# Kernel optimization log

Hardware: AMD Instinct MI355X
Metric: run time of the kernel (lower is better)

## Reference

```python
import jax, jax.numpy as jnp
import numpy as np

B, C, H, W = 512, 1, 128, 128
RS, WS = 12, 12
L, HID, T = 128, 512, 16


def setup_inputs() -> dict:
    key = jax.random.key(0)
    ks = jax.random.split(key, 24)

    def u(k, shape, fan):
        return jax.random.uniform(k, shape, jnp.float32, -1.0, 1.0) / np.sqrt(fan)

    enc_in = 2 * RS * RS + HID  # 800
    inp = {
        "x": jax.random.uniform(ks[0], (B, C, H, W), jnp.float32),
        "eps": jax.random.normal(ks[1], (T, B, L), jnp.float32),
        "glimpses": T,
        "canvas_init": jnp.zeros((C, H, W), jnp.float32),
        "h_dec_init": jnp.zeros((HID,), jnp.float32),
        "h_enc_init": jnp.zeros((HID,), jnp.float32),
        "W_ih_enc": u(ks[2], (4 * HID, enc_in), enc_in),
        "b_ih_enc": u(ks[3], (4 * HID,), enc_in),
        "W_hh_enc": u(ks[4], (4 * HID, HID), HID),
        "b_hh_enc": u(ks[5], (4 * HID,), HID),
        "W_ih_dec": u(ks[6], (4 * HID, L), L),
        "b_ih_dec": u(ks[7], (4 * HID,), L),
        "W_hh_dec": u(ks[8], (4 * HID, HID), HID),
        "b_hh_dec": u(ks[9], (4 * HID,), HID),
        "W_samp": u(ks[10], (2 * L, HID), HID),
        "b_samp": u(ks[11], (2 * L,), HID),
        "W_rattn": u(ks[12], (5, HID), HID),
        "b_rattn": u(ks[13], (5,), HID),
        "W_wattn": u(ks[14], (5, HID), HID),
        "b_wattn": u(ks[15], (5,), HID),
        "W_writer": u(ks[16], (WS * WS, HID), HID),
        "b_writer": u(ks[17], (WS * WS,), HID),
    }
    return inp


def _lstm_cell(x, h, c, Wih, bih, Whh, bhh):
    gates = x @ Wih.T + bih + h @ Whh.T + bhh
    i, f, g, o = jnp.split(gates, 4, axis=-1)
    c_new = jax.nn.sigmoid(f) * c + jax.nn.sigmoid(i) * jnp.tanh(g)
    h_new = jax.nn.sigmoid(o) * jnp.tanh(c_new)
    return h_new, c_new


def _filter_bank(gx, gy, variance, stride, size):
    # gx, gy, variance, stride: [B,1]
    offsets = (jnp.arange(size, dtype=jnp.float32) + 0.5 - size / 2) * stride  # [B,size]
    mu_x = (gx + offsets)[..., None]  # [B,size,1]
    mu_y = (gy + offsets)[..., None]
    var = variance[:, :, None]  # [B,1,1]
    a = jnp.arange(W, dtype=jnp.float32)
    b = jnp.arange(H, dtype=jnp.float32)
    Fx = jnp.exp(-((a - mu_x) ** 2) / (2 * var))  # [B,size,W]
    Fy = jnp.exp(-((b - mu_y) ** 2) / (2 * var))  # [B,size,H]
    Fx = Fx / jnp.maximum(Fx.sum(axis=2, keepdims=True), 1e-8)
    Fy = Fy / jnp.maximum(Fy.sum(axis=2, keepdims=True), 1e-8)
    return Fx, Fy


def _attn_window(h_state, Wattn, battn, size):
    res = h_state @ Wattn.T + battn  # [B,5]
    gx_, gy_, log_var, log_delta, log_inten = [res[:, i:i + 1] for i in range(5)]
    gx = (W + 1) * (gx_ + 1) / 2
    gy = (H + 1) * (gy_ + 1) / 2
    stride = (max(H, W) - 1) * jnp.exp(log_delta) / (size - 1)
    Fx, Fy = _filter_bank(gx, gy, jnp.exp(log_var), stride, size)
    return Fx, Fy, jnp.exp(log_inten)


def _read(x, x_error, h_dec, W_rattn, b_rattn):
    Fx, Fy, inten = _attn_window(h_dec, W_rattn, b_rattn, RS)
    FxT = jnp.swapaxes(Fx, -1, -2)[:, None]  # [B,1,W,RS]
    Fy = Fy[:, None]  # [B,1,RS,H]
    glimpse = jnp.concatenate((Fy @ x @ FxT, Fy @ x_error @ FxT), axis=1)  # [B,2C,RS,RS]
    return inten[:, :, None, None] * glimpse


def _write(h_dec, W_writer, b_writer, W_wattn, b_wattn):
    w = (h_dec @ W_writer.T + b_writer).reshape(-1, C, WS, WS)
    Fx, Fy, inten = _attn_window(h_dec, W_wattn, b_wattn, WS)
    FyT = jnp.swapaxes(Fy, -1, -2)[:, None]  # [B,1,H,WS]
    Fx = Fx[:, None]  # [B,1,WS,W]
    return (FyT @ w @ Fx) / inten[:, :, None, None]  # [B,C,H,W]


def reference(x, eps, glimpses, canvas_init, h_dec_init, h_enc_init,
              W_ih_enc, b_ih_enc, W_hh_enc, b_hh_enc,
              W_ih_dec, b_ih_dec, W_hh_dec, b_hh_dec,
              W_samp, b_samp, W_rattn, b_rattn, W_wattn, b_wattn,
              W_writer, b_writer):
    batch = x.shape[0]
    canvas0 = jnp.broadcast_to(canvas_init, (batch, C, H, W))
    h_dec0 = jnp.broadcast_to(h_dec_init, (batch, HID))
    h_enc0 = jnp.broadcast_to(h_enc_init, (batch, HID))
    c0 = jnp.zeros((batch, HID), x.dtype)

    def step(carry, eps_t):
        canvas, h_enc, c_enc, h_dec, c_dec = carry
        x_error = x - jax.nn.sigmoid(canvas)
        r = _read(x, x_error, h_dec, W_rattn, b_rattn).reshape(batch, -1)
        enc_in = jnp.concatenate((r, h_dec), axis=1)
        h_enc, c_enc = _lstm_cell(enc_in, h_enc, c_enc, W_ih_enc, b_ih_enc, W_hh_enc, b_hh_enc)
        s = h_enc @ W_samp.T + b_samp
        mu, log_var = s[:, :L], s[:, L:]
        z = mu + jnp.exp(log_var * 0.5) * eps_t
        h_dec, c_dec = _lstm_cell(z, h_dec, c_dec, W_ih_dec, b_ih_dec, W_hh_dec, b_hh_dec)
        canvas = canvas + _write(h_dec, W_writer, b_writer, W_wattn, b_wattn)
        return (canvas, h_enc, c_enc, h_dec, c_dec), (mu, log_var)

    (canvas, _, _, _, _), (mus, log_vars) = jax.lax.scan(
        step, (canvas0, h_enc0, c0, h_dec0, c0), eps[:glimpses])
    # mus/log_vars: [T,B,L] -> [B,T,L] to match torch.stack(mu, dim=1)
    return jax.nn.sigmoid(canvas), jnp.swapaxes(mus, 0, 1), jnp.swapaxes(log_vars, 0, 1)
```

## Files before the change

kernel.cpp:

```cpp
#include <hip/hip_runtime.h>
#include <hip/hip_bf16.h>
#include <math.h>

#define BATCH 512
#define HID 512
#define LAT 128
#define TSTEPS 16
#define IMG 16384
#define ENC_IN 800
#define GATES 2048

#define SEC_E 1344
#define SEC_D 640

typedef __attribute__((ext_vector_type(8))) short short8;
typedef __attribute__((ext_vector_type(4))) float f32x4;

__device__ __forceinline__ void gload16(const void* g, void* l) {
    __builtin_amdgcn_global_load_lds((const __attribute__((address_space(1))) unsigned int*)g,
                                     (__attribute__((address_space(3))) unsigned int*)l, 16, 0, 0);
}

__device__ __forceinline__ void bsplit(float v, unsigned short& hi, unsigned short& lo) {
    unsigned u = __float_as_uint(v);
    unsigned uh = (u + (0x7FFFu + ((u >> 16) & 1u))) & 0xFFFF0000u;
    hi = (unsigned short)(uh >> 16);
    float r = v - __uint_as_float(uh);
    unsigned ur = __float_as_uint(r);
    unsigned ul = (ur + (0x7FFFu + ((ur >> 16) & 1u))) & 0xFFFF0000u;
    lo = (unsigned short)(ul >> 16);
}

__global__ __launch_bounds__(256) void init_canvas(float* __restrict__ canvas,
                                                   const float* __restrict__ ci) {
    int idx = blockIdx.x * 256 + threadIdx.x;
    canvas[idx] = ci[idx & (IMG - 1)];
}

__global__ __launch_bounds__(256) void init_state(float* __restrict__ he, float* __restrict__ ce,
                                                  float* __restrict__ hd, float* __restrict__ cd,
                                                  const float* __restrict__ hei,
                                                  const float* __restrict__ hdi,
                                                  unsigned short* __restrict__ A_enc,
                                                  unsigned short* __restrict__ A_dec) {
    int idx = blockIdx.x * 256 + threadIdx.x;
    int b = idx >> 9, u = idx & 511;
    float ve = hei[u], vd = hdi[u];
    he[idx] = ve;
    hd[idx] = vd;
    ce[idx] = 0.f;
    cd[idx] = 0.f;
    unsigned short hi, lo;
    bsplit(ve, hi, lo);
    size_t be = (size_t)b * 2 * SEC_E;
    A_enc[be + 800 + u] = hi;
    A_enc[be + SEC_E + 800 + u] = lo;
    bsplit(vd, hi, lo);
    size_t bd = (size_t)b * 2 * SEC_D;
    A_dec[bd + 128 + u] = hi;
    A_dec[bd + SEC_D + 128 + u] = lo;
}

__global__ __launch_bounds__(256) void sigmoid_final(float* __restrict__ c) {
    int idx = blockIdx.x * 256 + threadIdx.x;
    c[idx] = 1.f / (1.f + expf(-c[idx]));
}

__global__ __launch_bounds__(256) void prep_wsplit(const float* __restrict__ W1, int K1,
                                                   const float* __restrict__ W2, int K2,
                                                   unsigned short* __restrict__ out, int SEC) {
    int kk = blockIdx.x * 256 + threadIdx.x;
    int n = blockIdx.y;
    if (kk >= SEC) return;
    float v = 0.f;
    if (kk < K1) v = W1[(size_t)n * K1 + kk];
    else if (kk < K1 + K2) v = W2[(size_t)n * K2 + (kk - K1)];
    unsigned short hi, lo;
    bsplit(v, hi, lo);
    size_t base = (size_t)n * 2 * SEC;
    out[base + kk] = hi;
    out[base + SEC + kk] = lo;
}

__global__ __launch_bounds__(256) void gemm_bf16x3(const unsigned short* __restrict__ Au,
                                                   const unsigned short* __restrict__ Wu,
                                                   float* __restrict__ C, int SEC,
                                                   int ktb0, int kte0, int ktb1, int kte1) {
    __shared__ __align__(16) char lds[2][16384];
    const __bf16* A = (const __bf16*)Au;
    const __bf16* Wt = (const __bf16*)Wu;
    const int ld = 2 * SEC;
    const int tid = threadIdx.x;
    const int z = blockIdx.z;
    const int bm = blockIdx.x * 64;
    const int bn = blockIdx.y * 64;
    const int ktb = z ? ktb1 : ktb0;
    const int kte = z ? kte1 : kte0;

    const int row0 = tid >> 3, c0 = tid & 7;
    const size_t ga0 = (size_t)(bm + row0) * ld + (size_t)((c0 ^ (row0 & 7)) * 8);
    const size_t ga1 = ga0 + (size_t)32 * ld;
    const size_t gb0 = (size_t)(bn + row0) * ld + (size_t)((c0 ^ (row0 & 7)) * 8);
    const size_t gb1 = gb0 + (size_t)32 * ld;
    const int lA0 = tid * 16, lA1 = (tid + 256) * 16;
    const int lB0 = 8192 + tid * 16, lB1 = 8192 + (tid + 256) * 16;

    const int lane = tid & 63, wv = tid >> 6;
    const int rA = wv * 16 + (lane & 15);
    const int chnk = (lane >> 4) ^ (lane & 7);
    const int byteA = rA * 128 + chnk * 16;
    const int byteB = 8192 + (lane & 15) * 128 + chnk * 16;

    f32x4 acc[4];
#pragma unroll
    for (int j = 0; j < 4; ++j) acc[j] = (f32x4){0.f, 0.f, 0.f, 0.f};

    auto STAGE = [&](int buf, int kt) {
        const int kw = kt * 64;
        const int ka = (kw >= SEC) ? (kw - SEC) : kw;
        const int kb = (kw >= 2 * SEC) ? (kw - 2 * SEC) : kw;
        const __bf16* a = A + ka;
        const __bf16* w = Wt + kb;
        char* l = &lds[buf][0];
        gload16(a + ga0, l + lA0);
        gload16(a + ga1, l + lA1);
        gload16(w + gb0, l + lB0);
        gload16(w + gb1, l + lB1);
    };

    STAGE(0, ktb);
    asm volatile("s_waitcnt vmcnt(0)" ::: "memory");
    __syncthreads();
    int buf = 0;
    for (int kt = ktb; kt < kte; ++kt) {
        if (kt + 1 < kte) STAGE(buf ^ 1, kt + 1);
        const char* base = &lds[buf][0];
        short8 a0 = *(const short8*)(base + byteA);
        short8 a1 = *(const short8*)(base + (byteA ^ 64));
#pragma unroll
        for (int j = 0; j < 4; ++j) {
            short8 b0 = *(const short8*)(base + (byteB + j * 2048));
            short8 b1 = *(const short8*)(base + ((byteB + j * 2048) ^ 64));
            acc[j] = __builtin_amdgcn_mfma_f32_16x16x32_bf16(a0, b0, acc[j], 0, 0, 0);
            acc[j] = __builtin_amdgcn_mfma_f32_16x16x32_bf16(a1, b1, acc[j], 0, 0, 0);
        }
        asm volatile("s_waitcnt vmcnt(0)" ::: "memory");
        __syncthreads();
        buf ^= 1;
    }
    float* Cz = C + (size_t)z * BATCH * GATES;
    const int crow = bm + wv * 16 + (lane >> 4) * 4;
    const int ccol = bn + (lane & 15);
#pragma unroll
    for (int j = 0; j < 4; ++j)
#pragma unroll
        for (int r = 0; r < 4; ++r)
            Cz[(size_t)(crow + r) * GATES + ccol + j * 16] = acc[j][r];
}

__global__ __launch_bounds__(512, 4) void read_glimpse_fused(const float* __restrict__ x,
                                                             const float* __restrict__ canvas,
                                                             const float* __restrict__ h_dec,
                                                             const float* __restrict__ Wa,
                                                             const float* __restrict__ ba,
                                                             unsigned short* __restrict__ A_enc) {
    const int b = blockIdx.x, t = threadIdx.x;
    __shared__ float par[5];
    __shared__ float fx[12][132], fy[12][132];
    __shared__ float dn[24];
    __shared__ float tm[12][132], te[12][132];
    __shared__ __align__(16) float pbuf[8][12][128];
    float* red = &pbuf[0][0][0];
    const float* hb = h_dec + (size_t)b * HID;
#pragma unroll
    for (int j = 0; j < 5; ++j) red[j * 512 + t] = hb[t] * Wa[j * HID + t];
    __syncthreads();
    for (int o = 256; o > 0; o >>= 1) {
        if (t < o) {
#pragma unroll
            for (int j = 0; j < 5; ++j) red[j * 512 + t] += red[j * 512 + t + o];
        }
        __syncthreads();
    }
    if (t < 5) par[t] = red[t * 512] + ba[t];
    __syncthreads();
    const float gx = 129.f * (par[0] + 1.f) * 0.5f;
    const float gy = 129.f * (par[1] + 1.f) * 0.5f;
    const float var = expf(par[2]);
    const float strd = 127.f * expf(par[3]) / 11.f;
    const float iv = expf(par[4]);
#pragma unroll
    for (int rep = 0; rep < 6; ++rep) {
        int e = t + rep * 512;
        int mat = e / 1536;
        int rr = (e - mat * 1536) >> 7;
        int cc = e & 127;
        float ctr = (mat ? gy : gx) + ((float)rr + 0.5f - 6.f) * strd;
        float d = (float)cc - ctr;
        float v = expf(-(d * d) / (2.f * var));
        float (*dst)[132] = mat ? fy : fx;
        dst[rr][cc] = v;
    }
    __syncthreads();
    if (t < 24) {
        const float (*src)[132] = (t < 12) ? fx : fy;
        int rr = (t < 12) ? t : t - 12;
        float s = 0.f;
        for (int k = 0; k < 128; ++k) s += src[rr][k];
        dn[t] = fmaxf(s, 1e-8f);
    }
    __syncthreads();
#pragma unroll
    for (int rep = 0; rep < 6; ++rep) {
        int e = t + rep * 512;
        int mat = e / 1536;
        int rr = (e - mat * 1536) >> 7;
        int cc = e & 127;
        float (*dst)[132] = mat ? fy : fx;
        dst[rr][cc] /= dn[mat * 12 + rr];
    }
    __syncthreads();
    const int g = t >> 6, l = t & 63, c2 = l * 2;
    float2 am[12] = {}, ae[12] = {};
    const float* xb = x + (size_t)b * IMG;
    const float* cb = canvas + (size_t)b * IMG;
    for (int hh = g * 16; hh < g * 16 + 16; ++hh) {
        float2 xv = *(const float2*)(xb + hh * 128 + c2);
        float2 cv = *(const float2*)(cb + hh * 128 + c2);
        float2 xe;
        xe.x = xv.x - 1.f / (1.f + expf(-cv.x));
        xe.y = xv.y - 1.f / (1.f + expf(-cv.y));
#pragma unroll
        for (int i = 0; i < 12; ++i) {
            float f = fy[i][hh];
            am[i].x += f * xv.x;
            am[i].y += f * xv.y;
            ae[i].x += f * xe.x;
            ae[i].y += f * xe.y;
        }
    }
#pragma unroll
    for (int i = 0; i < 12; ++i) *(float2*)(&pbuf[g][i][c2]) = am[i];
    __syncthreads();
    for (int it = t; it < 1536; it += 512) {
        int ii = it >> 7, cc = it & 127;
        float s = 0.f;
#pragma unroll
        for (int k = 0; k < 8; ++k) s += pbuf[k][ii][cc];
        tm[ii][cc] = s;
    }
    __syncthreads();
#pragma unroll
    for (int i = 0; i < 12; ++i) *(float2*)(&pbuf[g][i][c2]) = ae[i];
    __syncthreads();
    for (int it = t; it < 1536; it += 512) {
        int ii = it >> 7, cc = it & 127;
        float s = 0.f;
#pragma unroll
        for (int k = 0; k < 8; ++k) s += pbuf[k][ii][cc];
        te[ii][cc] = s;
    }
    __syncthreads();
    unsigned short hi, lo;
    unsigned short* rb = A_enc + (size_t)b * 2 * SEC_E;
    if (t < 288) {
        int ch = (t >= 144) ? 1 : 0;
        int rem = t - ch * 144;
        int ii = rem / 12, jj = rem - ii * 12;
        const float* src = ch ? te[ii] : tm[ii];
        float s = 0.f;
        for (int w2 = 0; w2 < 128; ++w2) s += src[w2] * fx[jj][w2];
        bsplit(iv * s, hi, lo);
        rb[t] = hi;
        rb[SEC_E + t] = lo;
    }
    bsplit(hb[t], hi, lo);
    rb[288 + t] = hi;
    rb[SEC_E + 288 + t] = lo;
    if (t < 32) {
        rb[1312 + t] = 0;
        rb[SEC_E + 1312 + t] = 0;
    }
}

template <int TM, int TN>
__global__ __launch_bounds__(256) void gemm_slab(const float* __restrict__ A0,
                                                 const float* __restrict__ W0,
                                                 const float* __restrict__ bias0, int ld0, int K0,
                                                 const float* __restrict__ A1,
                                                 const float* __restrict__ W1,
                                                 const float* __restrict__ bias1, int ld1, int K1,
                                                 float* __restrict__ C, int M, int N) {
    constexpr int BM = 16 * TM, BN = 16 * TN, BK = 16;
    __shared__ float As[BK][BM + 4];
    __shared__ float Ws[BK][BN + 4];
    const int z = blockIdx.z;
    const float* A = z ? A1 : A0;
    const float* Wm = z ? W1 : W0;
    const float* bs = z ? bias1 : bias0;
    const int ld = z ? ld1 : ld0;
    const int K = z ? K1 : K0;
    const int tid = threadIdx.x;
    const int tx = tid & 15, ty = tid >> 4;
    const int bm = blockIdx.x * BM, bn = blockIdx.y * BN;
    float acc[TM][TN] = {};
    for (int k0 = 0; k0 < K; k0 += BK) {
        __syncthreads();
        for (int i = tid; i < BM * 4; i += 256) {
            int row = i >> 2, c4 = i & 3;
            const float4 v = *(const float4*)(A + (size_t)(bm + row) * ld + k0 + c4 * 4);
            As[c4 * 4 + 0][row] = v.x;
            As[c4 * 4 + 1][row] = v.y;
            As[c4 * 4 + 2][row] = v.z;
            As[c4 * 4 + 3][row] = v.w;
        }
        for (int i = tid; i < BN * 4; i += 256) {
            int row = i >> 2, c4 = i & 3;
            int wr = bn + row;
            float4 v = make_float4(0.f, 0.f, 0.f, 0.f);
            if (wr < N) v = *(const float4*)(Wm + (size_t)wr * ld + k0 + c4 * 4);
            Ws[c4 * 4 + 0][row] = v.x;
            Ws[c4 * 4 + 1][row] = v.y;
            Ws[c4 * 4 + 2][row] = v.z;
            Ws[c4 * 4 + 3][row] = v.w;
        }
        __syncthreads();
#pragma unroll
        for (int c = 0; c < BK; ++c) {
            float a[TM], w[TN];
#pragma unroll
            for (int i = 0; i < TM; ++i) a[i] = As[c][ty * TM + i];
#pragma unroll
            for (int j = 0; j < TN; ++j) w[j] = Ws[c][tx * TN + j];
#pragma unroll
            for (int i = 0; i < TM; ++i)
#pragma unroll
                for (int j = 0; j < TN; ++j) acc[i][j] += a[i] * w[j];
        }
    }
    float* Cz = C + (size_t)z * M * N;
#pragma unroll
    for (int i = 0; i < TM; ++i) {
        const int rr = bm + ty * TM + i;
#pragma unroll
        for (int j = 0; j < TN; ++j) {
            const int cc = bn + tx * TN + j;
            if (cc < N) Cz[(size_t)rr * N + cc] = acc[i][j] + (bs ? bs[cc] : 0.f);
        }
    }
}

__global__ __launch_bounds__(256) void lstm_pw(const float* __restrict__ g0,
                                               const float* __restrict__ g1,
                                               const float* __restrict__ bih,
                                               const float* __restrict__ bhh,
                                               float* __restrict__ h, float* __restrict__ c,
                                               unsigned short* __restrict__ split_out,
                                               int soff, int SEC2) {
    int idx = blockIdx.x * 256 + threadIdx.x;
    int b = idx >> 9, u = idx & 511;
    size_t base = (size_t)b * GATES;
    float gi = g0[base + u] + g1[base + u] + bih[u] + bhh[u];
    float gf = g0[base + 512 + u] + g1[base + 512 + u] + bih[512 + u] + bhh[512 + u];
    float gg = g0[base + 1024 + u] + g1[base + 1024 + u] + bih[1024 + u] + bhh[1024 + u];
    float go = g0[base + 1536 + u] + g1[base + 1536 + u] + bih[1536 + u] + bhh[1536 + u];
    float si = 1.f / (1.f + expf(-gi));
    float sf = 1.f / (1.f + expf(-gf));
    float so = 1.f / (1.f + expf(-go));
    float cn = sf * c[idx] + si * tanhf(gg);
    c[idx] = cn;
    float hn = so * tanhf(cn);
    h[idx] = hn;
    unsigned short hi, lo;
    bsplit(hn, hi, lo);
    size_t sb = (size_t)b * 2 * SEC2;
    split_out[sb + soff + u] = hi;
    split_out[sb + SEC2 + soff + u] = lo;
}

__global__ __launch_bounds__(256) void z_kernel(const float* __restrict__ s,
                                                const float* __restrict__ eps_t,
                                                unsigned short* __restrict__ A_dec,
                                                float* __restrict__ mu_out,
                                                float* __restrict__ lv_out, int t) {
    int idx = blockIdx.x * 256 + threadIdx.x;
    int b = idx >> 7, l = idx & 127;
    int i0 = b * 256 + l;
    float mu = s[i0] + s[131072 + i0];
    float lv = s[i0 + 128] + s[131072 + i0 + 128];
    float zv = mu + expf(0.5f * lv) * eps_t[idx];
    unsigned short hi, lo;
    bsplit(zv, hi, lo);
    size_t bd = (size_t)b * 2 * SEC_D;
    A_dec[bd + l] = hi;
    A_dec[bd + SEC_D + l] = lo;
    size_t o = (size_t)b * (TSTEPS * LAT) + t * LAT + l;
    mu_out[o] = mu;
    lv_out[o] = lv;
}

__global__ __launch_bounds__(512, 4) void write_canvas_fused(float* __restrict__ canvas,
                                                             const float* __restrict__ h_dec,
                                                             const float* __restrict__ Wr,
                                                             const float* __restrict__ bwr,
                                                             const float* __restrict__ Wa,
                                                             const float* __restrict__ ba) {
    const int b = blockIdx.x, t = threadIdx.x;
    __shared__ float par[5];
    __shared__ float hl[512];
    __shared__ float red[5][512];
    __shared__ float fx[12][132], fyl[12][132];
    __shared__ float dn[24];
    __shared__ float wl[144];
    __shared__ float tl[128][13];
    const float* hb = h_dec + (size_t)b * HID;
    hl[t] = hb[t];
    __syncthreads();
#pragma unroll
    for (int j = 0; j < 5; ++j) red[j][t] = hl[t] * Wa[j * HID + t];
    __syncthreads();
    for (int o = 256; o > 0; o >>= 1) {
        if (t < o) {
#pragma unroll
            for (int j = 0; j < 5; ++j) red[j][t] += red[j][t + o];
        }
        __syncthreads();
    }
    if (t < 5) par[t] = red[t][0] + ba[t];
    __syncthreads();
    const float gx = 129.f * (par[0] + 1.f) * 0.5f;
    const float gy = 129.f * (par[1] + 1.f) * 0.5f;
    const float var = expf(par[2]);
    const float strd = 127.f * expf(par[3]) / 11.f;
    const float riv = 1.f / expf(par[4]);
#pragma unroll
    for (int rep = 0; rep < 6; ++rep) {
        int e = t + rep * 512;
        int mat = e / 1536;
        int rr = (e - mat * 1536) >> 7;
        int cc = e & 127;
        float ctr = (mat ? gy : gx) + ((float)rr + 0.5f - 6.f) * strd;
        float d = (float)cc - ctr;
        float v = expf(-(d * d) / (2.f * var));
        float (*dst)[132] = mat ? fyl : fx;
        dst[rr][cc] = v;
    }
    {
        const int wv = t >> 6, l = t & 63;
#pragma unroll
        for (int oi = 0; oi < 18; ++oi) {
            int o = wv * 18 + oi;
            float p = 0.f;
#pragma unroll
            for (int j = 0; j < 8; ++j) p += hl[l + 64 * j] * Wr[(size_t)o * 512 + l + 64 * j];
#pragma unroll
            for (int m = 32; m; m >>= 1) p += __shfl_xor(p, m, 64);
            if (l == 0) wl[o] = p + bwr[o];
        }
    }
    __syncthreads();
    if (t < 24) {
        const float (*src)[132] = (t < 12) ? fx : fyl;
        int rr = (t < 12) ? t : t - 12;
        float s = 0.f;
        for (int k = 0; k < 128; ++k) s += src[rr][k];
        dn[t] = fmaxf(s, 1e-8f);
    }
    __syncthreads();
#pragma unroll
    for (int rep = 0; rep < 6; ++rep) {
        int e = t + rep * 512;
        int mat = e / 1536;
        int rr = (e - mat * 1536) >> 7;
        int cc = e & 127;
        float (*dst)[132] = mat ? fyl : fx;
        dst[rr][cc] /= dn[mat * 12 + rr];
    }
    __syncthreads();
    if (t < 128) {
        float tj[12] = {};
#pragma unroll
        for (int i = 0; i < 12; ++i) {
            float f = fyl[i][t];
#pragma unroll
            for (int j = 0; j < 12; ++j) tj[j] += f * wl[i * 12 + j];
        }
#pragma unroll
        for (int j = 0; j < 12; ++j) tl[t][j] = tj[j];
    }
    __syncthreads();
    const int g = t >> 6, l = t & 63, c2 = l * 2;
    float* cb = canvas + (size_t)b * IMG;
    for (int hh = g * 16; hh < g * 16 + 16; ++hh) {
        float sx = 0.f, sy = 0.f;
#pragma unroll
        for (int j = 0; j < 12; ++j) {
            float tv = tl[hh][j];
            sx += tv * fx[j][c2];
            sy += tv * fx[j][c2 + 1];
        }
        float2 cv = *(float2*)(cb + hh * 128 + c2);
        cv.x += sx * riv;
        cv.y += sy * riv;
        *(float2*)(cb + hh * 128 + c2) = cv;
    }
}

extern "C" void kernel_launch(void* const* d_in, const int* in_sizes, int n_in,
                              void* d_out, int out_size, void* d_ws, size_t ws_size,
                              hipStream_t stream) {
    const float* x = (const float*)d_in[0];
    const float* eps = (const float*)d_in[1];
    const float* canvas_init = (const float*)d_in[3];
    const float* h_dec_init = (const float*)d_in[4];
    const float* h_enc_init = (const float*)d_in[5];
    const float* W_ih_enc = (const float*)d_in[6];
    const float* b_ih_enc = (const float*)d_in[7];
    const float* W_hh_enc = (const float*)d_in[8];
    const float* b_hh_enc = (const float*)d_in[9];
    const float* W_ih_dec = (const float*)d_in[10];
    const float* b_ih_dec = (const float*)d_in[11];
    const float* W_hh_dec = (const float*)d_in[12];
    const float* b_hh_dec = (const float*)d_in[13];
    const float* W_samp = (const float*)d_in[14];
    const float* b_samp = (const float*)d_in[15];
    const float* W_rattn = (const float*)d_in[16];
    const float* b_rattn = (const float*)d_in[17];
    const float* W_wattn = (const float*)d_in[18];
    const float* b_wattn = (const float*)d_in[19];
    const float* W_writer = (const float*)d_in[20];
    const float* b_writer = (const float*)d_in[21];

    float* out = (float*)d_out;
    float* canvas = out;
    float* out_mu = out + (size_t)BATCH * IMG;
    float* out_lv = out_mu + (size_t)BATCH * TSTEPS * LAT;

    float* ws = (float*)d_ws;
    size_t off = 0;
    auto alloc = [&](size_t n) { float* p = ws + off; off += n; return p; };
    float* h_enc = alloc((size_t)BATCH * HID);
    float* c_enc = alloc((size_t)BATCH * HID);
    float* h_dec = alloc((size_t)BATCH * HID);
    float* c_dec = alloc((size_t)BATCH * HID);
    float* gates = alloc((size_t)2 * BATCH * GATES);
    float* sbuf = alloc((size_t)2 * BATCH * 256);
    unsigned short* A_enc = (unsigned short*)alloc((size_t)BATCH * SEC_E);
    unsigned short* A_dec = (unsigned short*)alloc((size_t)BATCH * SEC_D);
    unsigned short* Ws_enc = (unsigned short*)alloc((size_t)GATES * SEC_E);
    unsigned short* Ws_dec = (unsigned short*)alloc((size_t)GATES * SEC_D);

    init_canvas<<<BATCH * IMG / 256, 256, 0, stream>>>(canvas, canvas_init);
    init_state<<<BATCH * HID / 256, 256, 0, stream>>>(h_enc, c_enc, h_dec, c_dec,
                                                      h_enc_init, h_dec_init, A_enc, A_dec);
    prep_wsplit<<<dim3((SEC_E + 255) / 256, GATES), 256, 0, stream>>>(W_ih_enc, ENC_IN, W_hh_enc, HID, Ws_enc, SEC_E);
    prep_wsplit<<<dim3((SEC_D + 255) / 256, GATES), 256, 0, stream>>>(W_ih_dec, LAT, W_hh_dec, HID, Ws_dec, SEC_D);

    const int ktE = 3 * SEC_E / 64;
    const int ktD = 3 * SEC_D / 64;

    for (int t = 0; t < TSTEPS; ++t) {
        read_glimpse_fused<<<BATCH, 512, 0, stream>>>(x, canvas, h_dec, W_rattn, b_rattn, A_enc);
        gemm_bf16x3<<<dim3(BATCH / 64, GATES / 64, 2), 256, 0, stream>>>(
            A_enc, Ws_enc, gates, SEC_E, 0, 32, 32, ktE);
        lstm_pw<<<BATCH * HID / 256, 256, 0, stream>>>(gates, gates + (size_t)BATCH * GATES,
                                                       b_ih_enc, b_hh_enc, h_enc, c_enc,
                                                       A_enc, 800, SEC_E);
        gemm_slab<4, 1><<<dim3(8, 16, 2), 256, 0, stream>>>(
            h_enc, W_samp, b_samp, HID, 256,
            h_enc + 256, W_samp + 256, nullptr, HID, 256, sbuf, BATCH, 256);
        z_kernel<<<BATCH * LAT / 256, 256, 0, stream>>>(sbuf, eps + (size_t)t * BATCH * LAT,
                                                        A_dec, out_mu, out_lv, t);
        gemm_bf16x3<<<dim3(BATCH / 64, GATES / 64, 2), 256, 0, stream>>>(
            A_dec, Ws_dec, gates, SEC_D, 0, 15, 15, ktD);
        lstm_pw<<<BATCH * HID / 256, 256, 0, stream>>>(gates, gates + (size_t)BATCH * GATES,
                                                       b_ih_dec, b_hh_dec, h_dec, c_dec,
                                                       A_dec, 128, SEC_D);
        write_canvas_fused<<<BATCH, 512, 0, stream>>>(canvas, h_dec, W_writer, b_writer,
                                                      W_wattn, b_wattn);
    }
    sigmoid_final<<<BATCH * IMG / 256, 256, 0, stream>>>(canvas);
}
```

Before: 1.962 ms.

## Fuse canvas write with next read, fuse enc LSTM with sampler and z

Merges each step's canvas write with the following step's glimpse read into one per-image kernel. The canvas is read and updated once, and x is consumed in the same pass, saving a full-canvas round trip per step. Also fuses the encoder LSTM pointwise stage with the sampler projection (using a pre-transposed W_samp) and the z reparameterisation. The final step folds the output sigmoid into the last write. This removes several launches and intermediate buffers per step, at the cost of larger kernels with heavy LDS use and lower occupancy.

Result: slower. 2.837 ms (+44.6%).

```diff
diff --git a/kernel.cpp b/kernel.cpp
--- a/kernel.cpp
+++ b/kernel.cpp
@@ -61,11 +61,6 @@
     A_dec[bd + SEC_D + 128 + u] = lo;
 }
 
-__global__ __launch_bounds__(256) void sigmoid_final(float* __restrict__ c) {
-    int idx = blockIdx.x * 256 + threadIdx.x;
-    c[idx] = 1.f / (1.f + expf(-c[idx]));
-}
-
 __global__ __launch_bounds__(256) void prep_wsplit(const float* __restrict__ W1, int K1,
                                                    const float* __restrict__ W2, int K2,
                                                    unsigned short* __restrict__ out, int SEC) {
@@ -82,6 +77,13 @@
     out[base + SEC + kk] = lo;
 }
 
+__global__ __launch_bounds__(256) void prep_wsampT(const float* __restrict__ W,
+                                                   float* __restrict__ WT) {
+    int i = blockIdx.x * 256 + threadIdx.x;
+    int o = i >> 9, k = i & 511;
+    WT[k * 256 + o] = W[o * 512 + k];
+}
+
 __global__ __launch_bounds__(256) void gemm_bf16x3(const unsigned short* __restrict__ Au,
                                                    const unsigned short* __restrict__ Wu,
                                                    float* __restrict__ C, int SEC,
@@ -283,70 +285,371 @@
     }
 }
 
-template <int TM, int TN>
-__global__ __launch_bounds__(256) void gemm_slab(const float* __restrict__ A0,
-                                                 const float* __restrict__ W0,
-                                                 const float* __restrict__ bias0, int ld0, int K0,
-                                                 const float* __restrict__ A1,
-                                                 const float* __restrict__ W1,
-                                                 const float* __restrict__ bias1, int ld1, int K1,
-                                                 float* __restrict__ C, int M, int N) {
-    constexpr int BM = 16 * TM, BN = 16 * TN, BK = 16;
-    __shared__ float As[BK][BM + 4];
-    __shared__ float Ws[BK][BN + 4];
-    const int z = blockIdx.z;
-    const float* A = z ? A1 : A0;
-    const float* Wm = z ? W1 : W0;
-    const float* bs = z ? bias1 : bias0;
-    const int ld = z ? ld1 : ld0;
-    const int K = z ? K1 : K0;
+__global__ __launch_bounds__(512, 2) void rw_canvas_fused(float* __restrict__ canvas,
+                                                          const float* __restrict__ x,
+                                                          const float* __restrict__ h_dec,
+                                                          const float* __restrict__ Wwa,
+                                                          const float* __restrict__ bwa,
+                                                          const float* __restrict__ Wwr,
+                                                          const float* __restrict__ bwr,
+                                                          const float* __restrict__ Wra,
+                                                          const float* __restrict__ bra,
+                                                          unsigned short* __restrict__ A_enc) {
+    const int b = blockIdx.x, t = threadIdx.x;
+    __shared__ float hl[512];
+    __shared__ float par[10];
+    __shared__ float fxw[12][132], fyw[12][132], fxr[12][132], fyr[12][132];
+    __shared__ float dn[48];
+    __shared__ float wl[144];
+    __shared__ float tl[128][13];
+    __shared__ float tm[12][132], te[12][132];
+    __shared__ __align__(16) float pbuf[8][12][128];
+    float* red = &pbuf[0][0][0];
+    hl[t] = h_dec[(size_t)b * HID + t];
+    __syncthreads();
+#pragma unroll
+    for (int j = 0; j < 5; ++j) {
+        red[j * 512 + t] = hl[t] * Wwa[j * HID + t];
+        red[(j + 5) * 512 + t] = hl[t] * Wra[j * HID + t];
+    }
+    __syncthreads();
+    for (int o = 256; o > 0; o >>= 1) {
+        if (t < o) {
+#pragma unroll
+            for (int j = 0; j < 10; ++j) red[j * 512 + t] += red[j * 512 + t + o];
+        }
+        __syncthreads();
+    }
+    if (t < 10) par[t] = red[t * 512] + ((t < 5) ? bwa[t] : bra[t - 5]);
+    __syncthreads();
+    const float gxw = 129.f * (par[0] + 1.f) * 0.5f;
+    const float gyw = 129.f * (par[1] + 1.f) * 0.5f;
+    const float varw = expf(par[2]);
+    const float strdw = 127.f * expf(par[3]) / 11.f;
+    const float riv = 1.f / expf(par[4]);
+    const float gxr = 129.f * (par[5] + 1.f) * 0.5f;
+    const float gyr = 129.f * (par[6] + 1.f) * 0.5f;
+    const float varr = expf(par[7]);
+    const float strdr = 127.f * expf(par[8]) / 11.f;
+    const float ivr = expf(par[9]);
+    {
+        const int wv = t >> 6, l = t & 63;
+#pragma unroll
+        for (int oi = 0; oi < 18; ++oi) {
+            int o = wv * 18 + oi;
+            float p = 0.f;
+#pragma unroll
+            for (int j = 0; j < 8; ++j) p += hl[l + 64 * j] * Wwr[(size_t)o * 512 + l + 64 * j];
+#pragma unroll
+            for (int m = 32; m; m >>= 1) p += __shfl_xor(p, m, 64);
+            if (l == 0) wl[o] = p + bwr[o];
+        }
+    }
+#pragma unroll
+    for (int rep = 0; rep < 12; ++rep) {
+        int e = t + rep * 512;
+        int mat = e / 1536;
+        int idx = e - mat * 1536;
+        int rr = idx >> 7, cc = idx & 127;
+        float g0 = (mat == 0) ? gxw : (mat == 1) ? gyw : (mat == 2) ? gxr : gyr;
+        float sd = (mat < 2) ? strdw : strdr;
+        float vv = (mat < 2) ? varw : varr;
+        float d = (float)cc - (g0 + ((float)rr + 0.5f - 6.f) * sd);
+        float v = expf(-(d * d) / (2.f * vv));
+        float* base = (mat == 0) ? &fxw[0][0] : (mat == 1) ? &fyw[0][0]
+                     : (mat == 2) ? &fxr[0][0] : &fyr[0][0];
+        base[rr * 132 + cc] = v;
+    }
+    __syncthreads();
+    if (t < 48) {
+        int mat = t / 12, rr = t - mat * 12;
+        const float* base = (mat == 0) ? &fxw[0][0] : (mat == 1) ? &fyw[0][0]
+                           : (mat == 2) ? &fxr[0][0] : &fyr[0][0];
+        float s = 0.f;
+        for (int k = 0; k < 128; ++k) s += base[rr * 132 + k];
+        dn[t] = fmaxf(s, 1e-8f);
+    }
+    __syncthreads();
+#pragma unroll
+    for (int rep = 0; rep < 12; ++rep) {
+        int e = t + rep * 512;
+        int mat = e / 1536;
+        int idx = e - mat * 1536;
+        int rr = idx >> 7, cc = idx & 127;
+        float* base = (mat == 0) ? &fxw[0][0] : (mat == 1) ? &fyw[0][0]
+                     : (mat == 2) ? &fxr[0][0] : &fyr[0][0];
+        base[rr * 132 + cc] /= dn[mat * 12 + rr];
+    }
+    __syncthreads();
+    if (t < 128) {
+        float tj[12] = {};
+#pragma unroll
+        for (int i = 0; i < 12; ++i) {
+            float f = fyw[i][t];
+#pragma unroll
+            for (int j = 0; j < 12; ++j) tj[j] += f * wl[i * 12 + j];
+        }
+#pragma unroll
+        for (int j = 0; j < 12; ++j) tl[t][j] = tj[j];
+    }
+    __syncthreads();
+    const int g = t >> 6, l = t & 63, c2 = l * 2;
+    float2 am[12] = {}, ae[12] = {};
+    const float* xb = x + (size_t)b * IMG;
+    float* cb = canvas + (size_t)b * IMG;
+    for (int hh = g * 16; hh < g * 16 + 16; ++hh) {
+        float sx = 0.f, sy = 0.f;
+#pragma unroll
+        for (int j = 0; j < 12; ++j) {
+            float tv = tl[hh][j];
+            sx += tv * fxw[j][c2];
+            sy += tv * fxw[j][c2 + 1];
+        }
+        float2 cv = *(float2*)(cb + hh * 128 + c2);
+        cv.x += sx * riv;
+        cv.y += sy * riv;
+        *(float2*)(cb + hh * 128 + c2) = cv;
+        float2 xv = *(const float2*)(xb + hh * 128 + c2);
+        float2 xe;
+        xe.x = xv.x - 1.f / (1.f + expf(-cv.x));
+        xe.y = xv.y - 1.f / (1.f + expf(-cv.y));
+#pragma unroll
+        for (int i = 0; i < 12; ++i) {
+            float f = fyr[i][hh];
+            am[i].x += f * xv.x;
+            am[i].y += f * xv.y;
+            ae[i].x += f * xe.x;
+            ae[i].y += f * xe.y;
+        }
+    }
+    __syncthreads();
+#pragma unroll
+    for (int i = 0; i < 12; ++i) *(float2*)(&pbuf[g][i][c2]) = am[i];
+    __syncthreads();
+    for (int it = t; it < 1536; it += 512) {
+        int ii = it >> 7, cc = it & 127;
+        float s = 0.f;
+#pragma unroll
+        for (int k = 0; k < 8; ++k) s += pbuf[k][ii][cc];
+        tm[ii][cc] = s;
+    }
+    __syncthreads();
+#pragma unroll
+    for (int i = 0; i < 12; ++i) *(float2*)(&pbuf[g][i][c2]) = ae[i];
+    __syncthreads();
+    for (int it = t; it < 1536; it += 512) {
+        int ii = it >> 7, cc = it & 127;
+        float s = 0.f;
+#pragma unroll
+        for (int k = 0; k < 8; ++k) s += pbuf[k][ii][cc];
+        te[ii][cc] = s;
+    }
+    __syncthreads();
+    unsigned short hi, lo;
+    unsigned short* rb = A_enc + (size_t)b * 2 * SEC_E;
+    if (t < 288) {
+        int ch = (t >= 144) ? 1 : 0;
+        int rem = t - ch * 144;
+        int ii = rem / 12, jj = rem - ii * 12;
+        const float* src = ch ? te[ii] : tm[ii];
+        float s = 0.f;
+        for (int w2 = 0; w2 < 128; ++w2) s += src[w2] * fxr[jj][w2];
+        bsplit(ivr * s, hi, lo);
+        rb[t] = hi;
+        rb[SEC_E + t] = lo;
+    }
+    bsplit(hl[t], hi, lo);
+    rb[288 + t] = hi;
+    rb[SEC_E + 288 + t] = lo;
+    if (t < 32) {
+        rb[1312 + t] = 0;
+        rb[SEC_E + 1312 + t] = 0;
+    }
+}
+
+__global__ __launch_bounds__(512, 4) void write_final_fused(float* __restrict__ canvas,
+                                                            const float* __restrict__ h_dec,
+                                                            const float* __restrict__ Wwa,
+                                                            const float* __restrict__ bwa,
+                                                            const float* __restrict__ Wwr,
+                                                            const float* __restrict__ bwr) {
+    const int b = blockIdx.x, t = threadIdx.x;
+    __shared__ float hl[512];
+    __shared__ float par[5];
+    __shared__ float red[5][512];
+    __shared__ float fx[12][132], fyl[12][132];
+    __shared__ float dn[24];
+    __shared__ float wl[144];
+    __shared__ float tl[128][13];
+    hl[t] = h_dec[(size_t)b * HID + t];
+    __syncthreads();
+#pragma unroll
+    for (int j = 0; j < 5; ++j) red[j][t] = hl[t] * Wwa[j * HID + t];
+    __syncthreads();
+    for (int o = 256; o > 0; o >>= 1) {
+        if (t < o) {
+#pragma unroll
+            for (int j = 0; j < 5; ++j) red[j][t] += red[j][t + o];
+        }
+        __syncthreads();
+    }
+    if (t < 5) par[t] = red[t][0] + bwa[t];
+    __syncthreads();
+    const float gx = 129.f * (par[0] + 1.f) * 0.5f;
+    const float gy = 129.f * (par[1] + 1.f) * 0.5f;
+    const float var = expf(par[2]);
+    const float strd = 127.f * expf(par[3]) / 11.f;
+    const float riv = 1.f / expf(par[4]);
+    {
+        const int wv = t >> 6, l = t & 63;
+#pragma unroll
+        for (int oi = 0; oi < 18; ++oi) {
+            int o = wv * 18 + oi;
+            float p = 0.f;
+#pragma unroll
+            for (int j = 0; j < 8; ++j) p += hl[l + 64 * j] * Wwr[(size_t)o * 512 + l + 64 * j];
+#pragma unroll
+            for (int m = 32; m; m >>= 1) p += __shfl_xor(p, m, 64);
+            if (l == 0) wl[o] = p + bwr[o];
+        }
+    }
+#pragma unroll
+    for (int rep = 0; rep < 6; ++rep) {
+        int e = t + rep * 512;
+        int mat = e / 1536;
+        int rr = (e - mat * 1536) >> 7;
+        int cc = e & 127;
+        float ctr = (mat ? gy : gx) + ((float)rr + 0.5f - 6.f) * strd;
+        float d = (float)cc - ctr;
+        float v = expf(-(d * d) / (2.f * var));
+        float (*dst)[132] = mat ? fyl : fx;
+        dst[rr][cc] = v;
+    }
+    __syncthreads();
+    if (t < 24) {
+        const float (*src)[132] = (t < 12) ? fx : fyl;
+        int rr = (t < 12) ? t : t - 12;
+        float s = 0.f;
+        for (int k = 0; k < 128; ++k) s += src[rr][k];
+        dn[t] = fmaxf(s, 1e-8f);
+    }
+    __syncthreads();
+#pragma unroll
+    for (int rep = 0; rep < 6; ++rep) {
+        int e = t + rep * 512;
+        int mat = e / 1536;
+        int rr = (e - mat * 1536) >> 7;
+        int cc = e & 127;
+        float (*dst)[132] = mat ? fyl : fx;
+        dst[rr][cc] /= dn[mat * 12 + rr];
+    }
+    __syncthreads();
+    if (t < 128) {
+        float tj[12] = {};
+#pragma unroll
+        for (int i = 0; i < 12; ++i) {
+            float f = fyl[i][t];
+#pragma unroll
+            for (int j = 0; j < 12; ++j) tj[j] += f * wl[i * 12 + j];
+        }
+#pragma unroll
+        for (int j = 0; j < 12; ++j) tl[t][j] = tj[j];
+    }
+    __syncthreads();
+    const int g = t >> 6, l = t & 63, c2 = l * 2;
+    float* cb = canvas + (size_t)b * IMG;
+    for (int hh = g * 16; hh < g * 16 + 16; ++hh) {
+        float sx = 0.f, sy = 0.f;
+#pragma unroll
+        for (int j = 0; j < 12; ++j) {
+            float tv = tl[hh][j];
+            sx += tv * fx[j][c2];
+            sy += tv * fx[j][c2 + 1];
+        }
+        float2 cv = *(float2*)(cb + hh * 128 + c2);
+        cv.x = 1.f / (1.f + expf(-(cv.x + sx * riv)));
+        cv.y = 1.f / (1.f + expf(-(cv.y + sy * riv)));
+        *(float2*)(cb + hh * 128 + c2) = cv;
+    }
+}
+
+__global__ __launch_bounds__(512, 2) void lstm_enc_samp_z(const float* __restrict__ g0,
+                                                          const float* __restrict__ g1,
+                                                          const float* __restrict__ bih,
+                                                          const float* __restrict__ bhh,
+                                                          float* __restrict__ h,
+                                                          float* __restrict__ c,
+                                                          unsigned short* __restrict__ A_enc,
+                                                          const float* __restrict__ WsT,
+                                                          const float* __restrict__ bs,
+                                                          const float* __restrict__ eps_t,
+                                                          unsigned short* __restrict__ A_dec,
+                                                          float* __restrict__ mu_out,
+                                                          float* __restrict__ lv_out, int t) {
+    const int bb = blockIdx.x * 4;
     const int tid = threadIdx.x;
-    const int tx = tid & 15, ty = tid >> 4;
-    const int bm = blockIdx.x * BM, bn = blockIdx.y * BN;
-    float acc[TM][TN] = {};
-    for (int k0 = 0; k0 < K; k0 += BK) {
-        __syncthreads();
-        for (int i = tid; i < BM * 4; i += 256) {
-            int row = i >> 2, c4 = i & 3;
-            const float4 v = *(const float4*)(A + (size_t)(bm + row) * ld + k0 + c4 * 4);
-            As[c4 * 4 + 0][row] = v.x;
-            As[c4 * 4 + 1][row] = v.y;
-            As[c4 * 4 + 2][row] = v.z;
-            As[c4 * 4 + 3][row] = v.w;
-        }
-        for (int i = tid; i < BN * 4; i += 256) {
-            int row = i >> 2, c4 = i & 3;
-            int wr = bn + row;
-            float4 v = make_float4(0.f, 0.f, 0.f, 0.f);
-            if (wr < N) v = *(const float4*)(Wm + (size_t)wr * ld + k0 + c4 * 4);
-            Ws[c4 * 4 + 0][row] = v.x;
-            Ws[c4 * 4 + 1][row] = v.y;
-            Ws[c4 * 4 + 2][row] = v.z;
-            Ws[c4 * 4 + 3][row] = v.w;
-        }
-        __syncthreads();
-#pragma unroll
-        for (int c = 0; c < BK; ++c) {
-            float a[TM], w[TN];
-#pragma unroll
-            for (int i = 0; i < TM; ++i) a[i] = As[c][ty * TM + i];
-#pragma unroll
-            for (int j = 0; j < TN; ++j) w[j] = Ws[c][tx * TN + j];
-#pragma unroll
-            for (int i = 0; i < TM; ++i)
-#pragma unroll
-                for (int j = 0; j < TN; ++j) acc[i][j] += a[i] * w[j];
-        }
-    }
-    float* Cz = C + (size_t)z * M * N;
-#pragma unroll
-    for (int i = 0; i < TM; ++i) {
-        const int rr = bm + ty * TM + i;
-#pragma unroll
-        for (int j = 0; j < TN; ++j) {
-            const int cc = bn + tx * TN + j;
-            if (cc < N) Cz[(size_t)rr * N + cc] = acc[i][j] + (bs ? bs[cc] : 0.f);
-        }
+    __shared__ float hl[4][512];
+    __shared__ float sred[2][4][256];
+    __shared__ float sfin[4][256];
+    unsigned short hi, lo;
+#pragma unroll
+    for (int q = 0; q < 4; ++q) {
+        const int b = bb + q, u = tid;
+        size_t base = (size_t)b * GATES;
+        float gi = g0[base + u] + g1[base + u] + bih[u] + bhh[u];
+        float gf = g0[base + 512 + u] + g1[base + 512 + u] + bih[512 + u] + bhh[512 + u];
+        float gg = g0[base + 1024 + u] + g1[base + 1024 + u] + bih[1024 + u] + bhh[1024 + u];
+        float go = g0[base + 1536 + u] + g1[base + 1536 + u] + bih[1536 + u] + bhh[1536 + u];
+        float si = 1.f / (1.f + expf(-gi));
+        float sf = 1.f / (1.f + expf(-gf));
+        float so = 1.f / (1.f + expf(-go));
+        size_t cidx = (size_t)b * HID + u;
+        float cn = sf * c[cidx] + si * tanhf(gg);
+        c[cidx] = cn;
+        float hn = so * tanhf(cn);
+        h[cidx] = hn;
+        hl[q][u] = hn;
+        bsplit(hn, hi, lo);
+        size_t sb = (size_t)b * 2 * SEC_E;
+        A_enc[sb + 800 + u] = hi;
+        A_enc[sb + SEC_E + 800 + u] = lo;
+    }
+    __syncthreads();
+    {
+        const int o = tid & 255, half = tid >> 8;
+        float p0 = 0.f, p1 = 0.f, p2 = 0.f, p3 = 0.f;
+        for (int k = half * 256; k < half * 256 + 256; ++k) {
+            float w = WsT[k * 256 + o];
+            p0 += hl[0][k] * w;
+            p1 += hl[1][k] * w;
+            p2 += hl[2][k] * w;
+            p3 += hl[3][k] * w;
+        }
+        sred[half][0][o] = p0;
+        sred[half][1][o] = p1;
+        sred[half][2][o] = p2;
+        sred[half][3][o] = p3;
+    }
+    __syncthreads();
+#pragma unroll
+    for (int r = 0; r < 2; ++r) {
+        int idx = tid + r * 512;
+        int q = idx >> 8, o = idx & 255;
+        sfin[q][o] = sred[0][q][o] + sred[1][q][o] + bs[o];
+    }
+    __syncthreads();
+    {
+        const int q = tid >> 7, l = tid & 127;
+        const int b = bb + q;
+        float mu = sfin[q][l], lv = sfin[q][l + 128];
+        float zv = mu + expf(0.5f * lv) * eps_t[(size_t)b * LAT + l];
+        bsplit(zv, hi, lo);
+        size_t bd = (size_t)b * 2 * SEC_D;
+        A_dec[bd + l] = hi;
+        A_dec[bd + SEC_D + l] = lo;
+        size_t o = (size_t)b * (TSTEPS * LAT) + t * LAT + l;
+        mu_out[o] = mu;
+        lv_out[o] = lv;
     }
 }
 
@@ -378,134 +681,6 @@
     split_out[sb + SEC2 + soff + u] = lo;
 }
 
-__global__ __launch_bounds__(256) void z_kernel(const float* __restrict__ s,
-                                                const float* __restrict__ eps_t,
-                                                unsigned short* __restrict__ A_dec,
-                                                float* __restrict__ mu_out,
-                                                float* __restrict__ lv_out, int t) {
-    int idx = blockIdx.x * 256 + threadIdx.x;
-    int b = idx >> 7, l = idx & 127;
-    int i0 = b * 256 + l;
-    float mu = s[i0] + s[131072 + i0];
-    float lv = s[i0 + 128] + s[131072 + i0 + 128];
-    float zv = mu + expf(0.5f * lv) * eps_t[idx];
-    unsigned short hi, lo;
-    bsplit(zv, hi, lo);
-    size_t bd = (size_t)b * 2 * SEC_D;
-    A_dec[bd + l] = hi;
-    A_dec[bd + SEC_D + l] = lo;
-    size_t o = (size_t)b * (TSTEPS * LAT) + t * LAT + l;
-    mu_out[o] = mu;
-    lv_out[o] = lv;
-}
-
-__global__ __launch_bounds__(512, 4) void write_canvas_fused(float* __restrict__ canvas,
-                                                             const float* __restrict__ h_dec,
-                                                             const float* __restrict__ Wr,
-                                                             const float* __restrict__ bwr,
-                                                             const float* __restrict__ Wa,
-                                                             const float* __restrict__ ba) {
-    const int b = blockIdx.x, t = threadIdx.x;
-    __shared__ float par[5];
-    __shared__ float hl[512];
-    __shared__ float red[5][512];
-    __shared__ float fx[12][132], fyl[12][132];
-    __shared__ float dn[24];
-    __shared__ float wl[144];
-    __shared__ float tl[128][13];
-    const float* hb = h_dec + (size_t)b * HID;
-    hl[t] = hb[t];
-    __syncthreads();
-#pragma unroll
-    for (int j = 0; j < 5; ++j) red[j][t] = hl[t] * Wa[j * HID + t];
-    __syncthreads();
-    for (int o = 256; o > 0; o >>= 1) {
-        if (t < o) {
-#pragma unroll
-            for (int j = 0; j < 5; ++j) red[j][t] += red[j][t + o];
-        }
-        __syncthreads();
-    }
-    if (t < 5) par[t] = red[t][0] + ba[t];
-    __syncthreads();
-    const float gx = 129.f * (par[0] + 1.f) * 0.5f;
-    const float gy = 129.f * (par[1] + 1.f) * 0.5f;
-    const float var = expf(par[2]);
-    const float strd = 127.f * expf(par[3]) / 11.f;
-    const float riv = 1.f / expf(par[4]);
-#pragma unroll
-    for (int rep = 0; rep < 6; ++rep) {
-        int e = t + rep * 512;
-        int mat = e / 1536;
-        int rr = (e - mat * 1536) >> 7;
-        int cc = e & 127;
-        float ctr = (mat ? gy : gx) + ((float)rr + 0.5f - 6.f) * strd;
-        float d = (float)cc - ctr;
-        float v = expf(-(d * d) / (2.f * var));
-        float (*dst)[132] = mat ? fyl : fx;
-        dst[rr][cc] = v;
-    }
-    {
-        const int wv = t >> 6, l = t & 63;
-#pragma unroll
-        for (int oi = 0; oi < 18; ++oi) {
-            int o = wv * 18 + oi;
-            float p = 0.f;
-#pragma unroll
-            for (int j = 0; j < 8; ++j) p += hl[l + 64 * j] * Wr[(size_t)o * 512 + l + 64 * j];
-#pragma unroll
-            for (int m = 32; m; m >>= 1) p += __shfl_xor(p, m, 64);
-            if (l == 0) wl[o] = p + bwr[o];
-        }
-    }
-    __syncthreads();
-    if (t < 24) {
-        const float (*src)[132] = (t < 12) ? fx : fyl;
-        int rr = (t < 12) ? t : t - 12;
-        float s = 0.f;
-        for (int k = 0; k < 128; ++k) s += src[rr][k];
-        dn[t] = fmaxf(s, 1e-8f);
-    }
-    __syncthreads();
-#pragma unroll
-    for (int rep = 0; rep < 6; ++rep) {
-        int e = t + rep * 512;
-        int mat = e / 1536;
-        int rr = (e - mat * 1536) >> 7;
-        int cc = e & 127;
-        float (*dst)[132] = mat ? fyl : fx;
-        dst[rr][cc] /= dn[mat * 12 + rr];
-    }
-    __syncthreads();
-    if (t < 128) {
-        float tj[12] = {};
-#pragma unroll
-        for (int i = 0; i < 12; ++i) {
-            float f = fyl[i][t];
-#pragma unroll
-            for (int j = 0; j < 12; ++j) tj[j] += f * wl[i * 12 + j];
-        }
-#pragma unroll
-        for (int j = 0; j < 12; ++j) tl[t][j] = tj[j];
-    }
-    __syncthreads();
-    const int g = t >> 6, l = t & 63, c2 = l * 2;
-    float* cb = canvas + (size_t)b * IMG;
-    for (int hh = g * 16; hh < g * 16 + 16; ++hh) {
-        float sx = 0.f, sy = 0.f;
-#pragma unroll
-        for (int j = 0; j < 12; ++j) {
-            float tv = tl[hh][j];
-            sx += tv * fx[j][c2];
-            sy += tv * fx[j][c2 + 1];
-        }
-        float2 cv = *(float2*)(cb + hh * 128 + c2);
-        cv.x += sx * riv;
-        cv.y += sy * riv;
-        *(float2*)(cb + hh * 128 + c2) = cv;
-    }
-}
-
 extern "C" void kernel_launch(void* const* d_in, const int* in_sizes, int n_in,
                               void* d_out, int out_size, void* d_ws, size_t ws_size,
                               hipStream_t stream) {
@@ -544,7 +719,7 @@
     float* h_dec = alloc((size_t)BATCH * HID);
     float* c_dec = alloc((size_t)BATCH * HID);
     float* gates = alloc((size_t)2 * BATCH * GATES);
-    float* sbuf = alloc((size_t)2 * BATCH * 256);
+    float* WsT = alloc((size_t)HID * 256);
     unsigned short* A_enc = (unsigned short*)alloc((size_t)BATCH * SEC_E);
     unsigned short* A_dec = (unsigned short*)alloc((size_t)BATCH * SEC_D);
     unsigned short* Ws_enc = (unsigned short*)alloc((size_t)GATES * SEC_E);
@@ -555,29 +730,31 @@
                                                       h_enc_init, h_dec_init, A_enc, A_dec);
     prep_wsplit<<<dim3((SEC_E + 255) / 256, GATES), 256, 0, stream>>>(W_ih_enc, ENC_IN, W_hh_enc, HID, Ws_enc, SEC_E);
     prep_wsplit<<<dim3((SEC_D + 255) / 256, GATES), 256, 0, stream>>>(W_ih_dec, LAT, W_hh_dec, HID, Ws_dec, SEC_D);
+    prep_wsampT<<<HID * 256 / 256, 256, 0, stream>>>(W_samp, WsT);
 
     const int ktE = 3 * SEC_E / 64;
     const int ktD = 3 * SEC_D / 64;
 
+    read_glimpse_fused<<<BATCH, 512, 0, stream>>>(x, canvas, h_dec, W_rattn, b_rattn, A_enc);
+
     for (int t = 0; t < TSTEPS; ++t) {
-        read_glimpse_fused<<<BATCH, 512, 0, stream>>>(x, canvas, h_dec, W_rattn, b_rattn, A_enc);
         gemm_bf16x3<<<dim3(BATCH / 64, GATES / 64, 2), 256, 0, stream>>>(
             A_enc, Ws_enc, gates, SEC_E, 0, 32, 32, ktE);
-        lstm_pw<<<BATCH * HID / 256, 256, 0, stream>>>(gates, gates + (size_t)BATCH * GATES,
-                                                       b_ih_enc, b_hh_enc, h_enc, c_enc,
-                                                       A_enc, 800, SEC_E);
-        gemm_slab<4, 1><<<dim3(8, 16, 2), 256, 0, stream>>>(
-            h_enc, W_samp, b_samp, HID, 256,
-            h_enc + 256, W_samp + 256, nullptr, HID, 256, sbuf, BATCH, 256);
-        z_kernel<<<BATCH * LAT / 256, 256, 0, stream>>>(sbuf, eps + (size_t)t * BATCH * LAT,
-                                                        A_dec, out_mu, out_lv, t);
+        lstm_enc_samp_z<<<BATCH / 4, 512, 0, stream>>>(
+            gates, gates + (size_t)BATCH * GATES, b_ih_enc, b_hh_enc, h_enc, c_enc, A_enc,
+            WsT, b_samp, eps + (size_t)t * BATCH * LAT, A_dec, out_mu, out_lv, t);
         gemm_bf16x3<<<dim3(BATCH / 64, GATES / 64, 2), 256, 0, stream>>>(
             A_dec, Ws_dec, gates, SEC_D, 0, 15, 15, ktD);
         lstm_pw<<<BATCH * HID / 256, 256, 0, stream>>>(gates, gates + (size_t)BATCH * GATES,
                                                        b_ih_dec, b_hh_dec, h_dec, c_dec,
                                                        A_dec, 128, SEC_D);
-        write_canvas_fused<<<BATCH, 512, 0, stream>>>(canvas, h_dec, W_writer, b_writer,
-                                                      W_wattn, b_wattn);
-    }
-    sigmoid_final<<<BATCH * IMG / 256, 256, 0, stream>>>(canvas);
-}
+        if (t < TSTEPS - 1) {
+            rw_canvas_fused<<<BATCH, 512, 0, stream>>>(canvas, x, h_dec,
+                                                       W_wattn, b_wattn, W_writer, b_writer,
+                                                       W_rattn, b_rattn, A_enc);
+        } else {
+            write_final_fused<<<BATCH, 512, 0, stream>>>(canvas, h_dec,
+                                                         W_wattn, b_wattn, W_writer, b_writer);
+        }
+    }
+}
```
